# Kernel tuning notes

Hardware: AMD Instinct MI355X
Metric: run time of the kernel (lower is better)

## Reference

```python
import jax, jax.numpy as jnp
import numpy as np

B, T, C, H, N = 4, 1024, 2048, 32, 64
DFF, DW, DV, DA, DG = 8192, 64, 32, 64, 128
GN_EPS = 64e-5  # RWKV7 ln_x GroupNorm eps


def _ln(x, w, b, eps=1e-5):
    m = x.mean(-1, keepdims=True)
    v = ((x - m) ** 2).mean(-1, keepdims=True)
    return (x - m) / jnp.sqrt(v + eps) * w + b


def _block(x, v_first, att_shift, ffn_shift, wkv_state,
           ln1_w, ln1_b, ln2_w, ln2_b,
           x_r, x_w, x_k, x_v, x_a, x_g,
           Wr, Wk, Wv, Wo,
           w0, w1, w2, v0, v1, v2, a0, a1, a2, g1, g2,
           k_k, k_a, r_k, lnx_w, lnx_b,
           ffn_xk, Wk_ffn, Wv_ffn):
    # ----- TimeMix -----
    xn = _ln(x, ln1_w, ln1_b)
    xx = jnp.concatenate([att_shift[:, None, :], xn[:, :-1]], axis=1) - xn
    xr = xn + xx * x_r
    xw = xn + xx * x_w
    xk_ = xn + xx * x_k
    xv = xn + xx * x_v
    xa = xn + xx * x_a
    xg = xn + xx * x_g

    r = xr @ Wr
    w = -jax.nn.softplus(-(w0 + jnp.tanh(xw @ w1) @ w2)) - 0.5  # <= -0.5
    k = xk_ @ Wk
    v = xv @ Wv
    # layer_id != 0: interpolate toward v_first
    v = v + (v_first - v) * jax.nn.sigmoid(v0 + (xv @ v1) @ v2)
    a = jax.nn.sigmoid(a0 + (xa @ a1) @ a2)
    g = jax.nn.sigmoid(xg @ g1) @ g2

    kk = (k * k_k).reshape(B, T, H, N)
    kk = kk / jnp.maximum(jnp.linalg.norm(kk, axis=-1, keepdims=True), 1e-12)
    k = k * (1.0 + (a - 1.0) * k_a)

    rh = r.reshape(B, T, H, N)
    wh = jnp.exp(-jnp.exp(w.reshape(B, T, H, N)))  # decay in (0,1)
    kh = k.reshape(B, T, H, N)
    vh = v.reshape(B, T, H, N)
    ah = a.reshape(B, T, H, N)
    aa = -kk
    bb = kk * ah

    def step(S, inp):
        # S: [B,H,N(value),N(key)]
        r_t, w_t, k_t, v_t, a_t, b_t = inp
        sa = jnp.einsum('bhvk,bhk->bhv', S, a_t)
        S = S * w_t[:, :, None, :] + sa[..., None] * b_t[:, :, None, :] + v_t[..., None] * k_t[:, :, None, :]
        y = jnp.einsum('bhvk,bhk->bhv', S, r_t)
        return S, y

    tm = lambda z: jnp.swapaxes(z, 0, 1)  # [B,T,H,N] -> [T,B,H,N]
    S_new, ys = jax.lax.scan(step, wkv_state, (tm(rh), tm(wh), tm(kh), tm(vh), tm(aa), tm(bb)))
    x_wkv = jnp.swapaxes(ys, 0, 1).reshape(B, T, C)

    # GroupNorm over H groups of size N (RWKV7 ln_x)
    xh = x_wkv.reshape(B, T, H, N)
    mu = xh.mean(-1, keepdims=True)
    var = ((xh - mu) ** 2).mean(-1, keepdims=True)
    x_wkv = ((xh - mu) / jnp.sqrt(var + GN_EPS)).reshape(B, T, C) * lnx_w + lnx_b

    resid = ((rh * kh * r_k).sum(-1, keepdims=True) * vh).reshape(B, T, C)
    x_wkv = x_wkv + resid
    att_out = (x_wkv * g) @ Wo
    x1 = x + att_out

    # ----- ChannelMix -----
    xn2 = _ln(x1, ln2_w, ln2_b)
    xx2 = jnp.concatenate([ffn_shift[:, None, :], xn2[:, :-1]], axis=1) - xn2
    xkf = xn2 + xx2 * ffn_xk
    kf = jnp.square(jax.nn.relu(xkf @ Wk_ffn))
    x_out = x1 + kf @ Wv_ffn
    return x_out, S_new


def setup_inputs() -> dict:
    ks = jax.random.split(jax.random.key(0), 48)
    rn = lambda i, sh, s=1.0: jax.random.normal(ks[i], sh, dtype=jnp.float32) * s
    return {
        'x': rn(0, (B, T, C)), 'v_first': rn(1, (B, T, C)),
        'att_shift': rn(2, (B, C)), 'ffn_shift': rn(3, (B, C)),
        'wkv_state': jnp.zeros((B, H, N, N), jnp.float32),
        'ln1_w': jnp.ones((C,), jnp.float32), 'ln1_b': jnp.zeros((C,), jnp.float32),
        'ln2_w': jnp.ones((C,), jnp.float32), 'ln2_b': jnp.zeros((C,), jnp.float32),
        'x_r': rn(4, (C,), 0.3), 'x_w': rn(5, (C,), 0.3), 'x_k': rn(6, (C,), 0.3),
        'x_v': rn(7, (C,), 0.3), 'x_a': rn(8, (C,), 0.3), 'x_g': rn(9, (C,), 0.3),
        'Wr': rn(10, (C, C), 0.02), 'Wk': rn(11, (C, C), 0.02),
        'Wv': rn(12, (C, C), 0.02), 'Wo': rn(13, (C, C), 0.02),
        'w0': rn(14, (C,), 0.3), 'w1': rn(15, (C, DW), 0.02), 'w2': rn(16, (DW, C), 0.02),
        'v0': rn(17, (C,), 0.3), 'v1': rn(18, (C, DV), 0.02), 'v2': rn(19, (DV, C), 0.02),
        'a0': rn(20, (C,), 0.3), 'a1': rn(21, (C, DA), 0.02), 'a2': rn(22, (DA, C), 0.02),
        'g1': rn(23, (C, DG), 0.02), 'g2': rn(24, (DG, C), 0.02),
        'k_k': rn(25, (C,), 0.1) + 0.7, 'k_a': rn(26, (C,), 0.1) + 0.7, 'r_k': rn(27, (H, N), 0.1),
        'lnx_w': jnp.ones((C,), jnp.float32), 'lnx_b': jnp.zeros((C,), jnp.float32),
        'ffn_xk': rn(28, (C,), 0.3), 'Wk_ffn': rn(29, (C, DFF), 0.02), 'Wv_ffn': rn(30, (DFF, C), 0.02),
    }


def reference(x, v_first, att_shift, ffn_shift, wkv_state,
              ln1_w, ln1_b, ln2_w, ln2_b,
              x_r, x_w, x_k, x_v, x_a, x_g,
              Wr, Wk, Wv, Wo,
              w0, w1, w2, v0, v1, v2, a0, a1, a2, g1, g2,
              k_k, k_a, r_k, lnx_w, lnx_b,
              ffn_xk, Wk_ffn, Wv_ffn):
    return _block(x, v_first, att_shift, ffn_shift, wkv_state,
                  ln1_w, ln1_b, ln2_w, ln2_b,
                  x_r, x_w, x_k, x_v, x_a, x_g,
                  Wr, Wk, Wv, Wo,
                  w0, w1, w2, v0, v1, v2, a0, a1, a2, g1, g2,
                  k_k, k_a, r_k, lnx_w, lnx_b,
                  ffn_xk, Wk_ffn, Wv_ffn)
```

## Files before the change

kernel.cpp:

```cpp
#include <hip/hip_runtime.h>
#include <cstdint>


typedef __attribute__((ext_vector_type(4))) float f32x4;
typedef __attribute__((ext_vector_type(8))) __bf16 bf16x8;
typedef __attribute__((ext_vector_type(8))) unsigned short us8;

#define DEV __device__ __forceinline__

DEV unsigned short f2b(float f) {
  union { float f; unsigned u; } v; v.f = f;
  unsigned r = v.u + 0x7fffu + ((v.u >> 16) & 1u);
  return (unsigned short)(r >> 16);
}
DEV float b2f(unsigned short u) {
  union { unsigned u; float f; } v; v.u = (unsigned)u << 16;
  return v.f;
}

DEV void gload16(const void* g, void* l) {
  void* gg = const_cast<void*>(g);
  __builtin_amdgcn_global_load_lds(
      (__attribute__((address_space(1))) unsigned int*)gg,
      (__attribute__((address_space(3))) unsigned int*)l, 16, 0, 0);
}

DEV float red8(float v) {
  v += __shfl_xor(v, 1);
  v += __shfl_xor(v, 2);
  v += __shfl_xor(v, 4);
  return v;
}


__global__ void k_transpose(const float* __restrict__ src,
                            unsigned short* __restrict__ dst, int R, int Cc) {
  __shared__ float tile[32][33];
  const int c0 = blockIdx.x * 32, r0 = blockIdx.y * 32;
  const int tx = threadIdx.x, ty = threadIdx.y;
  for (int i = ty; i < 32; i += 8)
    tile[i][tx] = src[(size_t)(r0 + i) * Cc + c0 + tx];
  __syncthreads();
  for (int i = ty; i < 32; i += 8)
    dst[(size_t)(c0 + i) * R + r0 + tx] = f2b(tile[tx][i]);
}

__global__ void k_wcat(const float* __restrict__ w1, const float* __restrict__ a1,
                       const float* __restrict__ v1, const float* __restrict__ g1,
                       const float* __restrict__ xw, const float* __restrict__ xa,
                       const float* __restrict__ xv, const float* __restrict__ xg,
                       unsigned short* __restrict__ dst) {
  const int i = blockIdx.x * 256 + threadIdx.x;
  if (i >= 384 * 4096) return;
  const int j = i >> 12, c = i & 4095;
  float val = 0.f;
  if (j < 288) {
    const float* W; const float* mix; int jj, D;
    if (j < 64)       { W = w1; mix = xw; jj = j;       D = 64;  }
    else if (j < 128) { W = a1; mix = xa; jj = j - 64;  D = 64;  }
    else if (j < 160) { W = v1; mix = xv; jj = j - 128; D = 32;  }
    else              { W = g1; mix = xg; jj = j - 160; D = 128; }
    const int cc = c & 2047;
    val = W[(size_t)cc * D + jj];
    if (c >= 2048) val *= mix[cc];
  }
  dst[i] = f2b(val);
}


DEV void breduce2(float& a, float& b, float* rbuf) {
#pragma unroll
  for (int m = 1; m < 64; m <<= 1) { a += __shfl_xor(a, m); b += __shfl_xor(b, m); }
  const int wid = threadIdx.x >> 6, lane = threadIdx.x & 63;
  if (lane == 0) { rbuf[wid] = a; rbuf[4 + wid] = b; }
  __syncthreads();
  a = rbuf[0] + rbuf[1] + rbuf[2] + rbuf[3];
  b = rbuf[4] + rbuf[5] + rbuf[6] + rbuf[7];
  __syncthreads();
}

__global__ __launch_bounds__(256)
void k_ln1_mix(const float* __restrict__ x, const float* __restrict__ shift,
               const float* __restrict__ lw, const float* __restrict__ lb,
               const float* __restrict__ mr, const float* __restrict__ mk,
               const float* __restrict__ mv,
               unsigned short* __restrict__ A2, unsigned short* __restrict__ xrb,
               unsigned short* __restrict__ xkb, unsigned short* __restrict__ xvb) {
  __shared__ float rbuf[8];
  const int m = blockIdx.x, tid = threadIdx.x;
  const int b = m >> 10, t = m & 1023;
  const float* xt = x + (size_t)m * 2048 + tid * 8;
  const float* xp = (t > 0) ? (x + (size_t)(m - 1) * 2048 + tid * 8)
                            : (shift + (size_t)b * 2048 + tid * 8);
  float vt[8], vp[8];
  *(float4*)&vt[0] = *(const float4*)(xt);
  *(float4*)&vt[4] = *(const float4*)(xt + 4);
  *(float4*)&vp[0] = *(const float4*)(xp);
  *(float4*)&vp[4] = *(const float4*)(xp + 4);
  float st = 0.f, sp = 0.f;
#pragma unroll
  for (int i = 0; i < 8; ++i) { st += vt[i]; sp += vp[i]; }
  breduce2(st, sp, rbuf);
  const float mt_ = st * (1.f / 2048.f), mp_ = sp * (1.f / 2048.f);
  float qt = 0.f, qp = 0.f;
#pragma unroll
  for (int i = 0; i < 8; ++i) {
    float d0 = vt[i] - mt_; qt += d0 * d0;
    float d1 = vp[i] - mp_; qp += d1 * d1;
  }
  breduce2(qt, qp, rbuf);
  const float rt = rsqrtf(qt * (1.f / 2048.f) + 1e-5f);
  const float rp = rsqrtf(qp * (1.f / 2048.f) + 1e-5f);
  const bool lnp = (t > 0);
#pragma unroll
  for (int i = 0; i < 8; ++i) {
    const int c = tid * 8 + i;
    const float wv = lw[c], bv = lb[c];
    const float xn = (vt[i] - mt_) * rt * wv + bv;
    const float pn = lnp ? ((vp[i] - mp_) * rp * wv + bv) : vp[i];
    const float xx = pn - xn;
    A2[(size_t)m * 4096 + c] = f2b(xn);
    A2[(size_t)m * 4096 + 2048 + c] = f2b(xx);
    xrb[(size_t)m * 2048 + c] = f2b(xn + xx * mr[c]);
    xkb[(size_t)m * 2048 + c] = f2b(xn + xx * mk[c]);
    xvb[(size_t)m * 2048 + c] = f2b(xn + xx * mv[c]);
  }
}

__global__ __launch_bounds__(256)
void k_ln2_mix(const float* __restrict__ x1, const float* __restrict__ shift,
               const float* __restrict__ lw, const float* __restrict__ lb,
               const float* __restrict__ mk, unsigned short* __restrict__ xkf) {
  __shared__ float rbuf[8];
  const int m = blockIdx.x, tid = threadIdx.x;
  const int b = m >> 10, t = m & 1023;
  const float* xt = x1 + (size_t)m * 2048 + tid * 8;
  const float* xp = (t > 0) ? (x1 + (size_t)(m - 1) * 2048 + tid * 8)
                            : (shift + (size_t)b * 2048 + tid * 8);
  float vt[8], vp[8];
  *(float4*)&vt[0] = *(const float4*)(xt);
  *(float4*)&vt[4] = *(const float4*)(xt + 4);
  *(float4*)&vp[0] = *(const float4*)(xp);
  *(float4*)&vp[4] = *(const float4*)(xp + 4);
  float st = 0.f, sp = 0.f;
#pragma unroll
  for (int i = 0; i < 8; ++i) { st += vt[i]; sp += vp[i]; }
  breduce2(st, sp, rbuf);
  const float mt_ = st * (1.f / 2048.f), mp_ = sp * (1.f / 2048.f);
  float qt = 0.f, qp = 0.f;
#pragma unroll
  for (int i = 0; i < 8; ++i) {
    float d0 = vt[i] - mt_; qt += d0 * d0;
    float d1 = vp[i] - mp_; qp += d1 * d1;
  }
  breduce2(qt, qp, rbuf);
  const float rt = rsqrtf(qt * (1.f / 2048.f) + 1e-5f);
  const float rp = rsqrtf(qp * (1.f / 2048.f) + 1e-5f);
  const bool lnp = (t > 0);
#pragma unroll
  for (int i = 0; i < 8; ++i) {
    const int c = tid * 8 + i;
    const float wv = lw[c], bv = lb[c];
    const float xn = (vt[i] - mt_) * rt * wv + bv;
    const float pn = lnp ? ((vp[i] - mp_) * rp * wv + bv) : vp[i];
    xkf[(size_t)m * 2048 + c] = f2b(xn + (pn - xn) * mk[c]);
  }
}


constexpr int EP_F32 = 0, EP_B16 = 1, EP_W = 2, EP_AB16 = 3, EP_VGB16 = 4,
              EP_RELU2 = 5, EP_ADDF = 6, EP_HACT = 7;

template <int EP>
DEV void ep_store(float acc, long row, long c, long ldc, float* Co,
                  unsigned short* Cob, const float* bias, const float* e0f,
                  const unsigned short* e0b) {
  const long idx = row * ldc + c;
  if constexpr (EP == EP_F32) {
    Co[idx] = acc;
  } else if constexpr (EP == EP_B16) {
    Cob[idx] = f2b(acc);
  } else if constexpr (EP == EP_W) {
    const float wv = bias[c] + acc;
    const float sp = log1pf(expf(-wv));
    const float w = -sp - 0.5f;
    Co[idx] = expf(-expf(w));
  } else if constexpr (EP == EP_AB16) {
    Cob[idx] = f2b(1.f / (1.f + expf(-(bias[c] + acc))));
  } else if constexpr (EP == EP_VGB16) {
    const float s = 1.f / (1.f + expf(-(bias[c] + acc)));
    const float vv = b2f(e0b[idx]);
    Cob[idx] = f2b(vv + (e0f[idx] - vv) * s);
  } else if constexpr (EP == EP_RELU2) {
    const float r = fmaxf(acc, 0.f);
    Cob[idx] = f2b(r * r);
  } else if constexpr (EP == EP_ADDF) {
    Co[idx] = acc + e0f[idx];
  } else if constexpr (EP == EP_HACT) {
    float vv = acc;
    if (c < 64) vv = tanhf(vv);
    else if (c >= 160) vv = 1.f / (1.f + expf(-vv));
    Cob[idx] = f2b(vv);
  }
}

template <int EP>
__global__ __launch_bounds__(256)
void gemm_bt(const unsigned short* __restrict__ A, long lda,
             const unsigned short* __restrict__ Bt, long ldb, long N, long K,
             long ldc, float* __restrict__ Co, unsigned short* __restrict__ Cob,
             const float* __restrict__ bias, const float* __restrict__ e0f,
             const unsigned short* __restrict__ e0b) {
  __shared__ unsigned short As[4096];
  __shared__ unsigned short Bs[4096];
  const int tid = threadIdx.x;
  const int wid = tid >> 6, lane = tid & 63;
  const long row0 = (long)blockIdx.x * 128, col0 = (long)blockIdx.y * 128;
  const int wm = (wid >> 1) * 64, wn = (wid & 1) * 64;
  f32x4 acc[4][4] = {};
  const int sr = tid >> 2, sk = (tid & 3) * 8;
  const unsigned short* gA = A + (row0 + sr) * lda + sk;
  const unsigned short* gB = Bt + (col0 + sr) * ldb + sk;
  unsigned short* lA = As + wid * 512;
  unsigned short* lB = Bs + wid * 512;
  const int fr = lane & 15, fk = (lane >> 4) * 8;

  for (long kb = 0; kb < K; kb += 32) {
    gload16(gA + kb, lA);
    gload16(gA + kb + 64 * lda, lA + 2048);
    gload16(gB + kb, lB);
    gload16(gB + kb + 64 * ldb, lB + 2048);
    __syncthreads();
    bf16x8 af[4], bq[4];
#pragma unroll
    for (int mt = 0; mt < 4; ++mt)
      af[mt] = *(const bf16x8*)(As + (wm + mt * 16 + fr) * 32 + fk);
#pragma unroll
    for (int nt = 0; nt < 4; ++nt)
      bq[nt] = *(const bf16x8*)(Bs + (wn + nt * 16 + fr) * 32 + fk);
#pragma unroll
    for (int mt = 0; mt < 4; ++mt)
#pragma unroll
      for (int nt = 0; nt < 4; ++nt)
        acc[mt][nt] = __builtin_amdgcn_mfma_f32_16x16x32_bf16(
            af[mt], bq[nt], acc[mt][nt], 0, 0, 0);
    __syncthreads();
  }
  const int fq = lane >> 4;
#pragma unroll
  for (int mt = 0; mt < 4; ++mt) {
#pragma unroll
    for (int nt = 0; nt < 4; ++nt) {
      const long c = col0 + wn + nt * 16 + fr;
      if (c < N) {
        const long rb = row0 + wm + mt * 16 + fq * 4;
#pragma unroll
        for (int rg = 0; rg < 4; ++rg)
          ep_store<EP>(acc[mt][nt][rg], rb + rg, c, ldc, Co, Cob, bias, e0f, e0b);
      }
    }
  }
}

__global__ __launch_bounds__(256)
void k_post(unsigned short* __restrict__ kio, unsigned short* __restrict__ abio,
            unsigned short* __restrict__ aao, const float* __restrict__ kkw,
            const float* __restrict__ kaw) {
  const int m = blockIdx.x, tid = threadIdx.x;
  const size_t base = (size_t)m * 2048 + tid * 8;
  us8 k8 = *(const us8*)(kio + base);
  us8 a8 = *(const us8*)(abio + base);
  float kk8[8], ka8[8];
  *(float4*)&kk8[0] = *(const float4*)(kkw + tid * 8);
  *(float4*)&kk8[4] = *(const float4*)(kkw + tid * 8 + 4);
  *(float4*)&ka8[0] = *(const float4*)(kaw + tid * 8);
  *(float4*)&ka8[4] = *(const float4*)(kaw + tid * 8 + 4);
  float kx[8], kv[8], av[8];
  float ss = 0.f;
#pragma unroll
  for (int i = 0; i < 8; ++i) {
    kv[i] = b2f(k8[i]); av[i] = b2f(a8[i]);
    kx[i] = kv[i] * kk8[i]; ss += kx[i] * kx[i];
  }
  ss = red8(ss);
  const float inv = 1.f / fmaxf(sqrtf(ss), 1e-12f);
  us8 kh8, aa8, bb8;
#pragma unroll
  for (int i = 0; i < 8; ++i) {
    const float kkn = kx[i] * inv;
    kh8[i] = f2b(kv[i] * (1.f + (av[i] - 1.f) * ka8[i]));
    aa8[i] = f2b(-kkn);
    bb8[i] = f2b(kkn * av[i]);
  }
  *(us8*)(kio + base) = kh8;
  *(us8*)(aao + base) = aa8;
  *(us8*)(abio + base) = bb8;
}


DEV float dpp3(float x) {
  union { float f; int i; } a, r;
  a.f = x; r.i = __builtin_amdgcn_update_dpp(0, a.i, 0xB1, 0xf, 0xf, true);
  x += r.f;
  a.f = x; r.i = __builtin_amdgcn_update_dpp(0, a.i, 0x4E, 0xf, 0xf, true);
  x += r.f;
  a.f = x; r.i = __builtin_amdgcn_update_dpp(0, a.i, 0x128, 0xf, 0xf, true);
  x += r.f;
  return x;
}

DEV void cv8(const uint4 q, float* o) {
  union { unsigned u; float f; } t;
  t.u = q.x << 16;          o[0] = t.f;
  t.u = q.x & 0xffff0000u;  o[1] = t.f;
  t.u = q.y << 16;          o[2] = t.f;
  t.u = q.y & 0xffff0000u;  o[3] = t.f;
  t.u = q.z << 16;          o[4] = t.f;
  t.u = q.z & 0xffff0000u;  o[5] = t.f;
  t.u = q.w << 16;          o[6] = t.f;
  t.u = q.w & 0xffff0000u;  o[7] = t.f;
}

__global__ __launch_bounds__(64)
void k_scan(const unsigned short* __restrict__ rp,
            const unsigned short* __restrict__ kp,
            const unsigned short* __restrict__ vp,
            const float* __restrict__ wp,
            const unsigned short* __restrict__ ap,
            const unsigned short* __restrict__ bp,
            const float* __restrict__ s0, float* __restrict__ yout,
            float* __restrict__ snew) {
  __shared__ float ylds[1024][8];
  const int lane = threadIdx.x;
  const int bh = blockIdx.x & 127;
  const int rq = blockIdx.x >> 7;
  const int b = bh >> 5, h = bh & 31;
  const int kg = (lane & 3) | ((lane >> 1) & 4);
  const int rl = ((lane >> 2) & 1) | ((lane >> 3) & 6);
  const int v = rq * 8 + rl, ks = kg * 8;
  const size_t off_bh = (size_t)b * 1024 * 2048 + (size_t)h * 64;

  const unsigned short* prb = rp + off_bh + ks;
  const unsigned short* pkb = kp + off_bh + ks;
  const unsigned short* pab = ap + off_bh + ks;
  const unsigned short* pbb = bp + off_bh + ks;
  const float*          pwb = wp + off_bh + ks;
  const unsigned short* pvb = vp + off_bh;

  float S[8];
  {
    const float* p = s0 + (((size_t)bh * 64 + v) * 64 + ks);
    *(float4*)&S[0] = *(const float4*)(p);
    *(float4*)&S[4] = *(const float4*)(p + 4);
  }

  uint4 r0_, k0_, a0_, b0_, r1_, k1_, a1_, b1_;
  uint4 r2_, k2_, a2_, b2_, r3_, k3_, a3_, b3_;
  float4 w00, w01, w10, w11, w20, w21, w30, w31;
  unsigned short vf0, vf1, vf2, vf3;

#define SCAN_LOAD(J, Br, Bk, Ba, Bb, Bw0, Bw1, Bvf, T)                       \
  {                                                                          \
    const size_t o_ = (size_t)(T) * 2048;                                    \
    Br = *(const uint4*)(prb + o_);   Bk = *(const uint4*)(pkb + o_);        \
    Ba = *(const uint4*)(pab + o_);   Bb = *(const uint4*)(pbb + o_);        \
    Bw0 = *(const float4*)(pwb + o_); Bw1 = *(const float4*)(pwb + o_ + 4);  \
    Bvf = pvb[o_ + v];                                                       \
  }

  SCAN_LOAD(0, r0_, k0_, a0_, b0_, w00, w01, vf0, 0)
  SCAN_LOAD(1, r1_, k1_, a1_, b1_, w10, w11, vf1, 1)
  SCAN_LOAD(2, r2_, k2_, a2_, b2_, w20, w21, vf2, 2)
  SCAN_LOAD(3, r3_, k3_, a3_, b3_, w30, w31, vf3, 3)

#define SCAN_BODY(T, Br, Bk, Ba, Bb, Bw0, Bw1, Bvf)                          \
  {                                                                          \
    float rr[8], kk[8], av[8], bv[8], wf[8];                                 \
    cv8(Br, rr); cv8(Bk, kk); cv8(Ba, av); cv8(Bb, bv);                      \
    *(float4*)&wf[0] = Bw0; *(float4*)&wf[4] = Bw1;                          \
    const float vv = b2f(Bvf);                                               \
    int tn_ = (T) + 4; if (tn_ > 1023) tn_ = 1023;                           \
    SCAN_LOAD(x, Br, Bk, Ba, Bb, Bw0, Bw1, Bvf, tn_)                         \
    float sa = 0.f;                                                          \
    _Pragma("unroll") for (int i = 0; i < 8; ++i) sa += S[i] * av[i];        \
    sa = dpp3(sa);                                                           \
    float y = 0.f;                                                           \
    _Pragma("unroll") for (int i = 0; i < 8; ++i) {                          \
      S[i] = S[i] * wf[i] + sa * bv[i] + vv * kk[i];                         \
      y += S[i] * rr[i];                                                     \
    }                                                                        \
    y = dpp3(y);                                                             \
    if (kg == 0) ylds[T][rl] = y;                                            \
  }

  for (int tb = 0; tb < 1024; tb += 4) {
    SCAN_BODY(tb + 0, r0_, k0_, a0_, b0_, w00, w01, vf0)
    SCAN_BODY(tb + 1, r1_, k1_, a1_, b1_, w10, w11, vf1)
    SCAN_BODY(tb + 2, r2_, k2_, a2_, b2_, w20, w21, vf2)
    SCAN_BODY(tb + 3, r3_, k3_, a3_, b3_, w30, w31, vf3)
  }
#undef SCAN_BODY
#undef SCAN_LOAD

  {
    float* p = snew + (((size_t)bh * 64 + v) * 64 + ks);
    *(float4*)(p) = *(const float4*)&S[0];
    *(float4*)(p + 4) = *(const float4*)&S[4];
  }
  __syncthreads();
#pragma unroll 4
  for (int it = 0; it < 32; ++it) {
    const int t = (lane >> 1) + it * 32;
    const int hf = (lane & 1) * 4;
    const float4 val = *(const float4*)&ylds[t][hf];
    *(float4*)(yout + off_bh + (size_t)t * 2048 + rq * 8 + hf) = val;
  }
}


__global__ __launch_bounds__(256)
void k_gn(const float* __restrict__ y, const unsigned short* __restrict__ r,
          const unsigned short* __restrict__ kh, const unsigned short* __restrict__ vf,
          const unsigned short* __restrict__ g, const float* __restrict__ rk,
          const float* __restrict__ lw, const float* __restrict__ lb,
          unsigned short* __restrict__ ywg) {
  const int m = blockIdx.x, tid = threadIdx.x;
  const size_t base = (size_t)m * 2048 + tid * 8;
  float yv[8];
  *(float4*)&yv[0] = *(const float4*)(y + base);
  *(float4*)&yv[4] = *(const float4*)(y + base + 4);
  us8 r8 = *(const us8*)(r + base);
  us8 k8 = *(const us8*)(kh + base);
  us8 v8 = *(const us8*)(vf + base);
  us8 g8 = *(const us8*)(g + base);
  float rkv[8];
  *(float4*)&rkv[0] = *(const float4*)(rk + tid * 8);
  *(float4*)&rkv[4] = *(const float4*)(rk + tid * 8 + 4);
  float sy = 0.f, sd = 0.f;
#pragma unroll
  for (int i = 0; i < 8; ++i) {
    sy += yv[i];
    sd += b2f(r8[i]) * b2f(k8[i]) * rkv[i];
  }
  sy = red8(sy);
  sd = red8(sd);
  const float mu = sy * (1.f / 64.f);
  float sq = 0.f;
#pragma unroll
  for (int i = 0; i < 8; ++i) { const float d = yv[i] - mu; sq += d * d; }
  sq = red8(sq);
  const float rstd = rsqrtf(sq * (1.f / 64.f) + 64e-5f);
  us8 o8;
#pragma unroll
  for (int i = 0; i < 8; ++i) {
    const int c = tid * 8 + i;
    const float gn = (yv[i] - mu) * rstd * lw[c] + lb[c];
    o8[i] = f2b((gn + sd * b2f(v8[i])) * b2f(g8[i]));
  }
  *(us8*)(ywg + base) = o8;
}


extern "C" void kernel_launch(void* const* d_in, const int* in_sizes, int n_in,
                              void* d_out, int out_size, void* d_ws,
                              size_t ws_size, hipStream_t stream) {
  (void)in_sizes; (void)n_in; (void)out_size; (void)ws_size;
  const float* x         = (const float*)d_in[0];
  const float* v_first   = (const float*)d_in[1];
  const float* att_shift = (const float*)d_in[2];
  const float* ffn_shift = (const float*)d_in[3];
  const float* wkv0      = (const float*)d_in[4];
  const float* ln1w = (const float*)d_in[5];
  const float* ln1b = (const float*)d_in[6];
  const float* ln2w = (const float*)d_in[7];
  const float* ln2b = (const float*)d_in[8];
  const float* x_r = (const float*)d_in[9];
  const float* x_w = (const float*)d_in[10];
  const float* x_k = (const float*)d_in[11];
  const float* x_v = (const float*)d_in[12];
  const float* x_a = (const float*)d_in[13];
  const float* x_g = (const float*)d_in[14];
  const float* Wr = (const float*)d_in[15];
  const float* Wk = (const float*)d_in[16];
  const float* Wv = (const float*)d_in[17];
  const float* Wo = (const float*)d_in[18];
  const float* w0 = (const float*)d_in[19];
  const float* w1 = (const float*)d_in[20];
  const float* w2 = (const float*)d_in[21];
  const float* v0 = (const float*)d_in[22];
  const float* v1 = (const float*)d_in[23];
  const float* v2 = (const float*)d_in[24];
  const float* a0 = (const float*)d_in[25];
  const float* a1 = (const float*)d_in[26];
  const float* a2 = (const float*)d_in[27];
  const float* g1 = (const float*)d_in[28];
  const float* g2 = (const float*)d_in[29];
  const float* k_k = (const float*)d_in[30];
  const float* k_a = (const float*)d_in[31];
  const float* r_k = (const float*)d_in[32];
  const float* lnxw = (const float*)d_in[33];
  const float* lnxb = (const float*)d_in[34];
  const float* ffn_xk = (const float*)d_in[35];
  const float* Wkf = (const float*)d_in[36];
  const float* Wvf = (const float*)d_in[37];

  char* ws = (char*)d_ws;
  constexpr size_t OFF_TWR   = 0;
  constexpr size_t OFF_TWK   = 8388608;
  constexpr size_t OFF_TWV   = 16777216;
  constexpr size_t OFF_TWO   = 25165824;
  constexpr size_t OFF_TW2   = 33554432;
  constexpr size_t OFF_TA2   = 33816576;
  constexpr size_t OFF_TV2   = 34078720;
  constexpr size_t OFF_TG2   = 34209792;
  constexpr size_t OFF_TWCAT = 34734080;
  constexpr size_t OFF_HACT  = 37879808;
  constexpr size_t OFF_GBUF  = 40239104;
  constexpr size_t OFF_WH    = 57016320;
  constexpr size_t OFF_R     = 90570752;
  constexpr size_t OFF_KH    = 107347968;
  constexpr size_t OFF_VF    = 124125184;
  constexpr size_t OFF_AA    = 140902400;
  constexpr size_t OFF_BB    = 157679616;

  unsigned short* tWr = (unsigned short*)(ws + OFF_TWR);
  unsigned short* tWk = (unsigned short*)(ws + OFF_TWK);
  unsigned short* tWv = (unsigned short*)(ws + OFF_TWV);
  unsigned short* tWo = (unsigned short*)(ws + OFF_TWO);
  unsigned short* tw2 = (unsigned short*)(ws + OFF_TW2);
  unsigned short* ta2 = (unsigned short*)(ws + OFF_TA2);
  unsigned short* tv2 = (unsigned short*)(ws + OFF_TV2);
  unsigned short* tg2 = (unsigned short*)(ws + OFF_TG2);
  unsigned short* tWcat = (unsigned short*)(ws + OFF_TWCAT);
  unsigned short* Hact  = (unsigned short*)(ws + OFF_HACT);
  unsigned short* gbuf  = (unsigned short*)(ws + OFF_GBUF);
  unsigned short* tWvfh = (unsigned short*)(ws + OFF_GBUF);
  unsigned short* act2  = (unsigned short*)(ws + OFF_WH);
  float*          whb   = (float*)(ws + OFF_WH);
  unsigned short* ywg   = (unsigned short*)(ws + OFF_WH);
  unsigned short* kf    = (unsigned short*)(ws + OFF_WH);
  unsigned short* bxr   = (unsigned short*)(ws + OFF_AA);
  unsigned short* bxk   = (unsigned short*)(ws + OFF_BB);
  unsigned short* bxv   = (unsigned short*)(ws + OFF_VF);
  unsigned short* rbuf  = (unsigned short*)(ws + OFF_R);
  unsigned short* khb   = (unsigned short*)(ws + OFF_KH);
  unsigned short* vfb   = (unsigned short*)(ws + OFF_VF);
  unsigned short* aab   = (unsigned short*)(ws + OFF_AA);
  unsigned short* bbb   = (unsigned short*)(ws + OFF_BB);
  unsigned short* vraw  = (unsigned short*)(ws + OFF_AA);
  unsigned short* abuf  = (unsigned short*)(ws + OFF_BB);
  float*          x1    = (float*)(ws + OFF_R);
  unsigned short* xkf   = (unsigned short*)(ws + OFF_VF);
  unsigned short* tWkf  = (unsigned short*)(ws + OFF_AA);
  float* out = (float*)d_out;
  float* snew = out + 8388608;

  const dim3 tb(32, 8);
  k_transpose<<<dim3(64, 64), tb, 0, stream>>>(Wr, tWr, 2048, 2048);
  k_transpose<<<dim3(64, 64), tb, 0, stream>>>(Wk, tWk, 2048, 2048);
  k_transpose<<<dim3(64, 64), tb, 0, stream>>>(Wv, tWv, 2048, 2048);
  k_transpose<<<dim3(64, 64), tb, 0, stream>>>(Wo, tWo, 2048, 2048);
  k_transpose<<<dim3(64, 2), tb, 0, stream>>>(w2, tw2, 64, 2048);
  k_transpose<<<dim3(64, 2), tb, 0, stream>>>(a2, ta2, 64, 2048);
  k_transpose<<<dim3(64, 1), tb, 0, stream>>>(v2, tv2, 32, 2048);
  k_transpose<<<dim3(64, 4), tb, 0, stream>>>(g2, tg2, 128, 2048);
  k_wcat<<<6144, 256, 0, stream>>>(w1, a1, v1, g1, x_w, x_a, x_v, x_g, tWcat);

  k_ln1_mix<<<4096, 256, 0, stream>>>(x, att_shift, ln1w, ln1b, x_r, x_k, x_v,
                                      act2, bxr, bxk, bxv);
  gemm_bt<EP_B16><<<dim3(32, 16), 256, 0, stream>>>(
      bxr, 2048, tWr, 2048, 2048, 2048, 2048, nullptr, rbuf, nullptr, nullptr, nullptr);
  gemm_bt<EP_B16><<<dim3(32, 16), 256, 0, stream>>>(
      bxk, 2048, tWk, 2048, 2048, 2048, 2048, nullptr, khb, nullptr, nullptr, nullptr);
  gemm_bt<EP_B16><<<dim3(32, 16), 256, 0, stream>>>(
      bxv, 2048, tWv, 2048, 2048, 2048, 2048, nullptr, vraw, nullptr, nullptr, nullptr);
  gemm_bt<EP_HACT><<<dim3(32, 3), 256, 0, stream>>>(
      act2, 4096, tWcat, 4096, 288, 4096, 288, nullptr, Hact, nullptr, nullptr, nullptr);
  gemm_bt<EP_W><<<dim3(32, 16), 256, 0, stream>>>(
      Hact + 0, 288, tw2, 64, 2048, 64, 2048, whb, nullptr, w0, nullptr, nullptr);
  gemm_bt<EP_AB16><<<dim3(32, 16), 256, 0, stream>>>(
      Hact + 64, 288, ta2, 64, 2048, 64, 2048, nullptr, abuf, a0, nullptr, nullptr);
  gemm_bt<EP_VGB16><<<dim3(32, 16), 256, 0, stream>>>(
      Hact + 128, 288, tv2, 32, 2048, 32, 2048, nullptr, vfb, v0, v_first, vraw);
  gemm_bt<EP_B16><<<dim3(32, 16), 256, 0, stream>>>(
      Hact + 160, 288, tg2, 128, 2048, 128, 2048, nullptr, gbuf, nullptr, nullptr, nullptr);
  k_post<<<4096, 256, 0, stream>>>(khb, abuf, aab, k_k, k_a);

  k_scan<<<1024, 64, 0, stream>>>(rbuf, khb, vfb, whb, aab, bbb, wkv0, out, snew);
  k_gn<<<4096, 256, 0, stream>>>(out, rbuf, khb, vfb, gbuf, r_k, lnxw, lnxb, ywg);

  gemm_bt<EP_ADDF><<<dim3(32, 16), 256, 0, stream>>>(
      ywg, 2048, tWo, 2048, 2048, 2048, 2048, x1, nullptr, nullptr, x, nullptr);

  k_ln2_mix<<<4096, 256, 0, stream>>>(x1, ffn_shift, ln2w, ln2b, ffn_xk, xkf);
  k_transpose<<<dim3(256, 64), tb, 0, stream>>>(Wkf, tWkf, 2048, 8192);
  gemm_bt<EP_RELU2><<<dim3(32, 32), 256, 0, stream>>>(
      xkf, 2048, tWkf, 2048, 4096, 2048, 4096, nullptr, kf, nullptr, nullptr, nullptr);
  k_transpose<<<dim3(64, 128), tb, 0, stream>>>(Wvf, tWvfh, 4096, 2048);
  gemm_bt<EP_ADDF><<<dim3(32, 16), 256, 0, stream>>>(
      kf, 4096, tWvfh, 4096, 2048, 4096, 2048, out, nullptr, nullptr, x1, nullptr);
  gemm_bt<EP_RELU2><<<dim3(32, 32), 256, 0, stream>>>(
      xkf, 2048, tWkf + (size_t)4096 * 2048, 2048, 4096, 2048, 4096, nullptr, kf,
      nullptr, nullptr, nullptr);
  k_transpose<<<dim3(64, 128), tb, 0, stream>>>(Wvf + (size_t)4096 * 2048, tWvfh,
                                                4096, 2048);
  gemm_bt<EP_ADDF><<<dim3(32, 16), 256, 0, stream>>>(
      kf, 4096, tWvfh, 4096, 2048, 4096, 2048, out, nullptr, nullptr, out, nullptr);
}
```

Measured before the change: 1.410 ms.

## Split WKV scan state across twice as many blocks with 4 keys per lane

The WKV scan kernel now gives each lane 4 key elements instead of 8 and 16 lanes per value row, so each 64-thread block handles 4 value rows and the grid doubles to 2048 blocks. The reductions gain one DPP step to sum across 16 lanes, and the prefetch depth grows from 4 to 8 timesteps. The intent is to shorten the per-step serial arithmetic chain and raise occupancy on the latency-bound recurrence. In exchange each block re-reads the r/k/a/b/w vectors, which doubles that redundant global traffic, and it adds a longer reduction.

```diff
diff --git a/kernel.cpp b/kernel.cpp
--- a/kernel.cpp
+++ b/kernel.cpp
@@ -298,27 +298,25 @@
 }
 
 
-DEV float dpp3(float x) {
+DEV float red16(float x) {
   union { float f; int i; } a, r;
   a.f = x; r.i = __builtin_amdgcn_update_dpp(0, a.i, 0xB1, 0xf, 0xf, true);
   x += r.f;
   a.f = x; r.i = __builtin_amdgcn_update_dpp(0, a.i, 0x4E, 0xf, 0xf, true);
   x += r.f;
+  a.f = x; r.i = __builtin_amdgcn_update_dpp(0, a.i, 0x124, 0xf, 0xf, true);
+  x += r.f;
   a.f = x; r.i = __builtin_amdgcn_update_dpp(0, a.i, 0x128, 0xf, 0xf, true);
   x += r.f;
   return x;
 }
 
-DEV void cv8(const uint4 q, float* o) {
+DEV void cv4(const uint2 q, float* o) {
   union { unsigned u; float f; } t;
   t.u = q.x << 16;          o[0] = t.f;
   t.u = q.x & 0xffff0000u;  o[1] = t.f;
   t.u = q.y << 16;          o[2] = t.f;
   t.u = q.y & 0xffff0000u;  o[3] = t.f;
-  t.u = q.z << 16;          o[4] = t.f;
-  t.u = q.z & 0xffff0000u;  o[5] = t.f;
-  t.u = q.w << 16;          o[6] = t.f;
-  t.u = q.w & 0xffff0000u;  o[7] = t.f;
 }
 
 __global__ __launch_bounds__(64)
@@ -330,14 +328,13 @@
             const unsigned short* __restrict__ bp,
             const float* __restrict__ s0, float* __restrict__ yout,
             float* __restrict__ snew) {
-  __shared__ float ylds[1024][8];
+  __shared__ float ylds[1024][4];
   const int lane = threadIdx.x;
   const int bh = blockIdx.x & 127;
   const int rq = blockIdx.x >> 7;
   const int b = bh >> 5, h = bh & 31;
-  const int kg = (lane & 3) | ((lane >> 1) & 4);
-  const int rl = ((lane >> 2) & 1) | ((lane >> 3) & 6);
-  const int v = rq * 8 + rl, ks = kg * 8;
+  const int kg = lane & 15, rl = lane >> 4;
+  const int v = rq * 4 + rl, ks = kg * 4;
   const size_t off_bh = (size_t)b * 1024 * 2048 + (size_t)h * 64;
 
   const unsigned short* prb = rp + off_bh + ks;
@@ -345,75 +342,74 @@
   const unsigned short* pab = ap + off_bh + ks;
   const unsigned short* pbb = bp + off_bh + ks;
   const float*          pwb = wp + off_bh + ks;
-  const unsigned short* pvb = vp + off_bh;
-
-  float S[8];
-  {
-    const float* p = s0 + (((size_t)bh * 64 + v) * 64 + ks);
-    *(float4*)&S[0] = *(const float4*)(p);
-    *(float4*)&S[4] = *(const float4*)(p + 4);
-  }
-
-  uint4 r0_, k0_, a0_, b0_, r1_, k1_, a1_, b1_;
-  uint4 r2_, k2_, a2_, b2_, r3_, k3_, a3_, b3_;
-  float4 w00, w01, w10, w11, w20, w21, w30, w31;
-  unsigned short vf0, vf1, vf2, vf3;
-
-#define SCAN_LOAD(J, Br, Bk, Ba, Bb, Bw0, Bw1, Bvf, T)                       \
+  const unsigned short* pvb = vp + off_bh + v;
+
+  float S[4];
+  *(float4*)&S[0] = *(const float4*)(s0 + (((size_t)bh * 64 + v) * 64 + ks));
+
+  uint2 r0_, k0_, a0_, b0_, r1_, k1_, a1_, b1_;
+  uint2 r2_, k2_, a2_, b2_, r3_, k3_, a3_, b3_;
+  uint2 r4_, k4_, a4_, b4_, r5_, k5_, a5_, b5_;
+  uint2 r6_, k6_, a6_, b6_, r7_, k7_, a7_, b7_;
+  float4 w0_, w1_, w2_, w3_, w4_, w5_, w6_, w7_;
+  unsigned short f0_, f1_, f2_, f3_, f4_, f5_, f6_, f7_;
+
+#define SLOAD(Br, Bk, Ba, Bb, Bw, Bf, T)                                     \
   {                                                                          \
     const size_t o_ = (size_t)(T) * 2048;                                    \
-    Br = *(const uint4*)(prb + o_);   Bk = *(const uint4*)(pkb + o_);        \
-    Ba = *(const uint4*)(pab + o_);   Bb = *(const uint4*)(pbb + o_);        \
-    Bw0 = *(const float4*)(pwb + o_); Bw1 = *(const float4*)(pwb + o_ + 4);  \
-    Bvf = pvb[o_ + v];                                                       \
-  }
-
-  SCAN_LOAD(0, r0_, k0_, a0_, b0_, w00, w01, vf0, 0)
-  SCAN_LOAD(1, r1_, k1_, a1_, b1_, w10, w11, vf1, 1)
-  SCAN_LOAD(2, r2_, k2_, a2_, b2_, w20, w21, vf2, 2)
-  SCAN_LOAD(3, r3_, k3_, a3_, b3_, w30, w31, vf3, 3)
-
-#define SCAN_BODY(T, Br, Bk, Ba, Bb, Bw0, Bw1, Bvf)                          \
+    Br = *(const uint2*)(prb + o_);  Bk = *(const uint2*)(pkb + o_);         \
+    Ba = *(const uint2*)(pab + o_);  Bb = *(const uint2*)(pbb + o_);         \
+    Bw = *(const float4*)(pwb + o_); Bf = pvb[o_];                           \
+  }
+
+  SLOAD(r0_, k0_, a0_, b0_, w0_, f0_, 0)
+  SLOAD(r1_, k1_, a1_, b1_, w1_, f1_, 1)
+  SLOAD(r2_, k2_, a2_, b2_, w2_, f2_, 2)
+  SLOAD(r3_, k3_, a3_, b3_, w3_, f3_, 3)
+  SLOAD(r4_, k4_, a4_, b4_, w4_, f4_, 4)
+  SLOAD(r5_, k5_, a5_, b5_, w5_, f5_, 5)
+  SLOAD(r6_, k6_, a6_, b6_, w6_, f6_, 6)
+  SLOAD(r7_, k7_, a7_, b7_, w7_, f7_, 7)
+
+#define SBODY(T, Br, Bk, Ba, Bb, Bw, Bf)                                     \
   {                                                                          \
-    float rr[8], kk[8], av[8], bv[8], wf[8];                                 \
-    cv8(Br, rr); cv8(Bk, kk); cv8(Ba, av); cv8(Bb, bv);                      \
-    *(float4*)&wf[0] = Bw0; *(float4*)&wf[4] = Bw1;                          \
-    const float vv = b2f(Bvf);                                               \
-    int tn_ = (T) + 4; if (tn_ > 1023) tn_ = 1023;                           \
-    SCAN_LOAD(x, Br, Bk, Ba, Bb, Bw0, Bw1, Bvf, tn_)                         \
-    float sa = 0.f;                                                          \
-    _Pragma("unroll") for (int i = 0; i < 8; ++i) sa += S[i] * av[i];        \
-    sa = dpp3(sa);                                                           \
-    float y = 0.f;                                                           \
-    _Pragma("unroll") for (int i = 0; i < 8; ++i) {                          \
-      S[i] = S[i] * wf[i] + sa * bv[i] + vv * kk[i];                         \
-      y += S[i] * rr[i];                                                     \
-    }                                                                        \
-    y = dpp3(y);                                                             \
+    float rr[4], kk[4], av[4], bv[4];                                        \
+    cv4(Br, rr); cv4(Bk, kk); cv4(Ba, av); cv4(Bb, bv);                      \
+    const float4 wf = Bw;                                                    \
+    const float vv = b2f(Bf);                                                \
+    int tn_ = (T) + 8; if (tn_ > 1023) tn_ = 1023;                           \
+    SLOAD(Br, Bk, Ba, Bb, Bw, Bf, tn_)                                       \
+    float sa = S[0] * av[0] + S[1] * av[1] + S[2] * av[2] + S[3] * av[3];    \
+    sa = red16(sa);                                                          \
+    float y;                                                                 \
+    S[0] = S[0] * wf.x + sa * bv[0] + vv * kk[0]; y  = S[0] * rr[0];         \
+    S[1] = S[1] * wf.y + sa * bv[1] + vv * kk[1]; y += S[1] * rr[1];         \
+    S[2] = S[2] * wf.z + sa * bv[2] + vv * kk[2]; y += S[2] * rr[2];         \
+    S[3] = S[3] * wf.w + sa * bv[3] + vv * kk[3]; y += S[3] * rr[3];         \
+    y = red16(y);                                                            \
     if (kg == 0) ylds[T][rl] = y;                                            \
   }
 
-  for (int tb = 0; tb < 1024; tb += 4) {
-    SCAN_BODY(tb + 0, r0_, k0_, a0_, b0_, w00, w01, vf0)
-    SCAN_BODY(tb + 1, r1_, k1_, a1_, b1_, w10, w11, vf1)
-    SCAN_BODY(tb + 2, r2_, k2_, a2_, b2_, w20, w21, vf2)
-    SCAN_BODY(tb + 3, r3_, k3_, a3_, b3_, w30, w31, vf3)
-  }
-#undef SCAN_BODY
-#undef SCAN_LOAD
-
-  {
-    float* p = snew + (((size_t)bh * 64 + v) * 64 + ks);
-    *(float4*)(p) = *(const float4*)&S[0];
-    *(float4*)(p + 4) = *(const float4*)&S[4];
-  }
+  for (int tb = 0; tb < 1024; tb += 8) {
+    SBODY(tb + 0, r0_, k0_, a0_, b0_, w0_, f0_)
+    SBODY(tb + 1, r1_, k1_, a1_, b1_, w1_, f1_)
+    SBODY(tb + 2, r2_, k2_, a2_, b2_, w2_, f2_)
+    SBODY(tb + 3, r3_, k3_, a3_, b3_, w3_, f3_)
+    SBODY(tb + 4, r4_, k4_, a4_, b4_, w4_, f4_)
+    SBODY(tb + 5, r5_, k5_, a5_, b5_, w5_, f5_)
+    SBODY(tb + 6, r6_, k6_, a6_, b6_, w6_, f6_)
+    SBODY(tb + 7, r7_, k7_, a7_, b7_, w7_, f7_)
+  }
+#undef SBODY
+#undef SLOAD
+
+  *(float4*)(snew + (((size_t)bh * 64 + v) * 64 + ks)) = *(const float4*)&S[0];
   __syncthreads();
 #pragma unroll 4
-  for (int it = 0; it < 32; ++it) {
-    const int t = (lane >> 1) + it * 32;
-    const int hf = (lane & 1) * 4;
-    const float4 val = *(const float4*)&ylds[t][hf];
-    *(float4*)(yout + off_bh + (size_t)t * 2048 + rq * 8 + hf) = val;
+  for (int it = 0; it < 16; ++it) {
+    const int t = lane + it * 64;
+    *(float4*)(yout + off_bh + (size_t)t * 2048 + rq * 4) =
+        *(const float4*)&ylds[t][0];
   }
 }
 
@@ -586,7 +582,7 @@
       Hact + 160, 288, tg2, 128, 2048, 128, 2048, nullptr, gbuf, nullptr, nullptr, nullptr);
   k_post<<<4096, 256, 0, stream>>>(khb, abuf, aab, k_k, k_a);
 
-  k_scan<<<1024, 64, 0, stream>>>(rbuf, khb, vfb, whb, aab, bbb, wkv0, out, snew);
+  k_scan<<<2048, 64, 0, stream>>>(rbuf, khb, vfb, whb, aab, bbb, wkv0, out, snew);
   k_gn<<<4096, 256, 0, stream>>>(out, rbuf, khb, vfb, gbuf, r_k, lnxw, lnxb, ywg);
 
   gemm_bt<EP_ADDF><<<dim3(32, 16), 256, 0, stream>>>(
```

After: 1.416 ms. Within noise of the previous version (+0.4%).
